# Kernel tuning notes

Hardware: AMD Instinct MI355X
Metric: run time of the kernel (lower is better)

Reference implementation:

```python
import jax, jax.numpy as jnp
import numpy as np

N, M, D = 8192, 8192, 64

def softplus(x):
    # transform_forward in pmf-automl
    return jnp.logaddexp(x, 0.0)

def inv_softplus(y):
    # transform_backward: log(exp(y) - 1), stable form
    return y + jnp.log(-jnp.expm1(-y))

def setup_inputs() -> dict:
    key = jax.random.key(0)
    k1, k2 = jax.random.split(key)
    X = jax.random.normal(k1, (N, D), dtype=jnp.float32)
    X2 = jax.random.normal(k2, (M, D), dtype=jnp.float32)
    # raw (pre-softplus) parameters, matching torch init: softplus(raw)=1
    lengthscale = jnp.full((1, D), inv_softplus(jnp.float32(1.0)), dtype=jnp.float32)
    variance = jnp.full((1,), inv_softplus(jnp.float32(1.0)), dtype=jnp.float32)
    return {"X": X, "X2": X2, "lengthscale": lengthscale, "variance": variance}

def reference(X, X2, lengthscale, variance):
    l = softplus(lengthscale)           # [1, D]
    v = softplus(variance)              # [1]
    Xl = X / l                          # [N, D]
    X2l = X2 / l                        # [M, D]
    xn = jnp.sum(Xl * Xl, axis=1)       # [N]
    yn = jnp.sum(X2l * X2l, axis=1)     # [M]
    cross = Xl @ X2l.T                  # [N, M]
    d2 = jnp.maximum(xn[:, None] + yn[None, :] - 2.0 * cross, 0.0)
    return v[0] * jnp.exp(-0.5 * d2)
```

## Files before the change

### kernel.cpp

```cpp
#include <hip/hip_runtime.h>
#include <math.h>

#define NN 8192
#define MM 8192
#define DD 64
#define BM 128
#define BN 128
#define LDS_S 132

__device__ __forceinline__ float softplus_f(float x) {
    return fmaxf(x, 0.0f) + log1pf(exp2f(-fabsf(x) * 1.4426950408889634f));
}

__global__ __launch_bounds__(256, 2)
void rbf_tile_kernel(const float* __restrict__ X, const float* __restrict__ X2,
                     const float* __restrict__ raw_l, const float* __restrict__ raw_v,
                     float* __restrict__ out) {
    __shared__ float As[DD][LDS_S];
    __shared__ float Bs[DD][LDS_S];
    __shared__ float xn[BM];
    __shared__ float yn[BN];

    const int t  = threadIdx.x;
    const int bn = blockIdx.x;
    const int bm = blockIdx.y;

    const int k4 = t & 15;
    const int r0 = t >> 4;

    float4 rl = ((const float4*)raw_l)[k4];
    const float il0 = 1.0f / softplus_f(rl.x);
    const float il1 = 1.0f / softplus_f(rl.y);
    const float il2 = 1.0f / softplus_f(rl.z);
    const float il3 = 1.0f / softplus_f(rl.w);

    const float* Xb  = X  + (size_t)(bm * BM) * DD;
    const float* X2b = X2 + (size_t)(bn * BN) * DD;

#pragma unroll
    for (int r = 0; r < 8; ++r) {
        const int row = r0 + 16 * r;
        float4 a = *(const float4*)(Xb + row * DD + 4 * k4);
        As[4 * k4 + 0][row] = a.x * il0;
        As[4 * k4 + 1][row] = a.y * il1;
        As[4 * k4 + 2][row] = a.z * il2;
        As[4 * k4 + 3][row] = a.w * il3;
        float4 b = *(const float4*)(X2b + row * DD + 4 * k4);
        Bs[4 * k4 + 0][row] = b.x * il0;
        Bs[4 * k4 + 1][row] = b.y * il1;
        Bs[4 * k4 + 2][row] = b.z * il2;
        Bs[4 * k4 + 3][row] = b.w * il3;
    }
    __syncthreads();

    {
        const int c = t & 127;
        float s = 0.0f;
        if (t < 128) {
#pragma unroll
            for (int k = 0; k < DD; ++k) { float a = As[k][c]; s = fmaf(a, a, s); }
            xn[c] = s;
        } else {
#pragma unroll
            for (int k = 0; k < DD; ++k) { float b = Bs[k][c]; s = fmaf(b, b, s); }
            yn[c] = s;
        }
    }
    __syncthreads();

    const int tx = t & 15;
    const int ty = t >> 4;

    float acc[2][4][2][4];
#pragma unroll
    for (int ii = 0; ii < 2; ++ii)
#pragma unroll
        for (int i = 0; i < 4; ++i)
#pragma unroll
            for (int jj = 0; jj < 2; ++jj)
#pragma unroll
                for (int j = 0; j < 4; ++j) acc[ii][i][jj][j] = 0.0f;

#pragma unroll 4
    for (int k = 0; k < DD; ++k) {
        float4 a0 = *(const float4*)&As[k][4 * ty];
        float4 a1 = *(const float4*)&As[k][4 * ty + 64];
        float4 b0 = *(const float4*)&Bs[k][4 * tx];
        float4 b1 = *(const float4*)&Bs[k][4 * tx + 64];
        float a[2][4] = {{a0.x, a0.y, a0.z, a0.w}, {a1.x, a1.y, a1.z, a1.w}};
        float b[2][4] = {{b0.x, b0.y, b0.z, b0.w}, {b1.x, b1.y, b1.z, b1.w}};
#pragma unroll
        for (int ii = 0; ii < 2; ++ii)
#pragma unroll
            for (int i = 0; i < 4; ++i)
#pragma unroll
                for (int jj = 0; jj < 2; ++jj)
#pragma unroll
                    for (int j = 0; j < 4; ++j)
                        acc[ii][i][jj][j] = fmaf(a[ii][i], b[jj][j], acc[ii][i][jj][j]);
    }

    const float v = softplus_f(raw_v[0]);
    const float c_exp = -0.5f * 1.4426950408889634f;

#pragma unroll
    for (int ii = 0; ii < 2; ++ii) {
#pragma unroll
        for (int i = 0; i < 4; ++i) {
            const int m = 4 * ty + 64 * ii + i;
            const float xnm = xn[m];
            float* orow = out + (size_t)(bm * BM + m) * MM + bn * BN;
#pragma unroll
            for (int jj = 0; jj < 2; ++jj) {
                const int n0 = 4 * tx + 64 * jj;
                float4 o;
                {
                    float d2 = fmaxf(xnm + yn[n0 + 0] - 2.0f * acc[ii][i][jj][0], 0.0f);
                    o.x = v * exp2f(c_exp * d2);
                }
                {
                    float d2 = fmaxf(xnm + yn[n0 + 1] - 2.0f * acc[ii][i][jj][1], 0.0f);
                    o.y = v * exp2f(c_exp * d2);
                }
                {
                    float d2 = fmaxf(xnm + yn[n0 + 2] - 2.0f * acc[ii][i][jj][2], 0.0f);
                    o.z = v * exp2f(c_exp * d2);
                }
                {
                    float d2 = fmaxf(xnm + yn[n0 + 3] - 2.0f * acc[ii][i][jj][3], 0.0f);
                    o.w = v * exp2f(c_exp * d2);
                }
                *(float4*)(orow + n0) = o;
            }
        }
    }
}

extern "C" void kernel_launch(void* const* d_in, const int* in_sizes, int n_in,
                              void* d_out, int out_size, void* d_ws, size_t ws_size,
                              hipStream_t stream) {
    const float* X     = (const float*)d_in[0];
    const float* X2    = (const float*)d_in[1];
    const float* raw_l = (const float*)d_in[2];
    const float* raw_v = (const float*)d_in[3];
    float* out = (float*)d_out;

    dim3 grid(MM / BN, NN / BM);
    dim3 block(256);
    rbf_tile_kernel<<<grid, block, 0, stream>>>(X, X2, raw_l, raw_v, out);
}
```

Before: 356.3 us.

## Compute cross term with split-bf16 MFMA instead of fp32 FMA

Replaces the scalar fp32 outer-product GEMM with bf16 MFMA 16x16x32 instructions. Operands are split into hi and lo bf16 parts and three products are accumulated to keep accuracy close to fp32. Row norms are now computed in fp32 straight from global memory, and the output layout changes to per-lane scalar stores. This trades 3x MFMA work and narrower, less coalesced stores for matrix-core throughput. The kernel is likely bound by the 256MB output write, so the gain may be limited.

```diff
diff --git a/kernel.cpp b/kernel.cpp
--- a/kernel.cpp
+++ b/kernel.cpp
@@ -6,18 +6,25 @@
 #define DD 64
 #define BM 128
 #define BN 128
-#define LDS_S 132
+#define STR 72
+
+typedef __bf16 bf16x8 __attribute__((ext_vector_type(8)));
+typedef __bf16 bf16x4 __attribute__((ext_vector_type(4)));
+typedef float f32x4 __attribute__((ext_vector_type(4)));
 
 __device__ __forceinline__ float softplus_f(float x) {
     return fmaxf(x, 0.0f) + log1pf(exp2f(-fabsf(x) * 1.4426950408889634f));
 }
 
 __global__ __launch_bounds__(256, 2)
-void rbf_tile_kernel(const float* __restrict__ X, const float* __restrict__ X2,
+void rbf_mfma_kernel(const float* __restrict__ X, const float* __restrict__ X2,
                      const float* __restrict__ raw_l, const float* __restrict__ raw_v,
                      float* __restrict__ out) {
-    __shared__ float As[DD][LDS_S];
-    __shared__ float Bs[DD][LDS_S];
+    __shared__ __bf16 Ah[BM][STR];
+    __shared__ __bf16 Al[BM][STR];
+    __shared__ __bf16 Bh[BN][STR];
+    __shared__ __bf16 Bl[BN][STR];
+    __shared__ float ls[DD];
     __shared__ float xn[BM];
     __shared__ float yn[BN];
 
@@ -25,14 +32,15 @@
     const int bn = blockIdx.x;
     const int bm = blockIdx.y;
 
+    if (t < DD) ls[t] = 1.0f / softplus_f(raw_l[t]);
+    __syncthreads();
+
     const int k4 = t & 15;
     const int r0 = t >> 4;
-
-    float4 rl = ((const float4*)raw_l)[k4];
-    const float il0 = 1.0f / softplus_f(rl.x);
-    const float il1 = 1.0f / softplus_f(rl.y);
-    const float il2 = 1.0f / softplus_f(rl.z);
-    const float il3 = 1.0f / softplus_f(rl.w);
+    const float il0 = ls[4 * k4 + 0];
+    const float il1 = ls[4 * k4 + 1];
+    const float il2 = ls[4 * k4 + 2];
+    const float il3 = ls[4 * k4 + 3];
 
     const float* Xb  = X  + (size_t)(bm * BM) * DD;
     const float* X2b = X2 + (size_t)(bn * BN) * DD;
@@ -40,97 +48,99 @@
 #pragma unroll
     for (int r = 0; r < 8; ++r) {
         const int row = r0 + 16 * r;
-        float4 a = *(const float4*)(Xb + row * DD + 4 * k4);
-        As[4 * k4 + 0][row] = a.x * il0;
-        As[4 * k4 + 1][row] = a.y * il1;
-        As[4 * k4 + 2][row] = a.z * il2;
-        As[4 * k4 + 3][row] = a.w * il3;
-        float4 b = *(const float4*)(X2b + row * DD + 4 * k4);
-        Bs[4 * k4 + 0][row] = b.x * il0;
-        Bs[4 * k4 + 1][row] = b.y * il1;
-        Bs[4 * k4 + 2][row] = b.z * il2;
-        Bs[4 * k4 + 3][row] = b.w * il3;
+        {
+            float4 a = *(const float4*)(Xb + row * DD + 4 * k4);
+            a.x *= il0; a.y *= il1; a.z *= il2; a.w *= il3;
+            bf16x4 h, l;
+            h[0] = (__bf16)a.x; l[0] = (__bf16)(a.x - (float)h[0]);
+            h[1] = (__bf16)a.y; l[1] = (__bf16)(a.y - (float)h[1]);
+            h[2] = (__bf16)a.z; l[2] = (__bf16)(a.z - (float)h[2]);
+            h[3] = (__bf16)a.w; l[3] = (__bf16)(a.w - (float)h[3]);
+            *(bf16x4*)&Ah[row][4 * k4] = h;
+            *(bf16x4*)&Al[row][4 * k4] = l;
+        }
+        {
+            float4 b = *(const float4*)(X2b + row * DD + 4 * k4);
+            b.x *= il0; b.y *= il1; b.z *= il2; b.w *= il3;
+            bf16x4 h, l;
+            h[0] = (__bf16)b.x; l[0] = (__bf16)(b.x - (float)h[0]);
+            h[1] = (__bf16)b.y; l[1] = (__bf16)(b.y - (float)h[1]);
+            h[2] = (__bf16)b.z; l[2] = (__bf16)(b.z - (float)h[2]);
+            h[3] = (__bf16)b.w; l[3] = (__bf16)(b.w - (float)h[3]);
+            *(bf16x4*)&Bh[row][4 * k4] = h;
+            *(bf16x4*)&Bl[row][4 * k4] = l;
+        }
+    }
+
+    {
+        const int rowl = t & 127;
+        const float* p = (t < 128) ? (Xb + rowl * DD) : (X2b + rowl * DD);
+        float s = 0.0f;
+#pragma unroll
+        for (int j = 0; j < 16; ++j) {
+            float4 a = *(const float4*)(p + 4 * j);
+            float e;
+            e = a.x * ls[4 * j + 0]; s = fmaf(e, e, s);
+            e = a.y * ls[4 * j + 1]; s = fmaf(e, e, s);
+            e = a.z * ls[4 * j + 2]; s = fmaf(e, e, s);
+            e = a.w * ls[4 * j + 3]; s = fmaf(e, e, s);
+        }
+        if (t < 128) xn[rowl] = s; else yn[rowl] = s;
     }
     __syncthreads();
 
-    {
-        const int c = t & 127;
-        float s = 0.0f;
-        if (t < 128) {
+    const int lane = t & 63;
+    const int q    = lane >> 4;
+    const int r16  = lane & 15;
+    const int w    = t >> 6;
+    const int row0 = (w >> 1) * 64;
+    const int col0 = (w & 1) * 64;
+
+    f32x4 acc[4][4];
 #pragma unroll
-            for (int k = 0; k < DD; ++k) { float a = As[k][c]; s = fmaf(a, a, s); }
-            xn[c] = s;
-        } else {
+    for (int mi = 0; mi < 4; ++mi)
 #pragma unroll
-            for (int k = 0; k < DD; ++k) { float b = Bs[k][c]; s = fmaf(b, b, s); }
-            yn[c] = s;
+        for (int ni = 0; ni < 4; ++ni)
+#pragma unroll
+            for (int r = 0; r < 4; ++r) acc[mi][ni][r] = 0.0f;
+
+#pragma unroll
+    for (int kc = 0; kc < 2; ++kc) {
+        const int k0 = kc * 32 + q * 8;
+        bf16x8 ah[4], al[4], bh[4], bl[4];
+#pragma unroll
+        for (int i = 0; i < 4; ++i) {
+            ah[i] = *(const bf16x8*)&Ah[row0 + i * 16 + r16][k0];
+            al[i] = *(const bf16x8*)&Al[row0 + i * 16 + r16][k0];
+            bh[i] = *(const bf16x8*)&Bh[col0 + i * 16 + r16][k0];
+            bl[i] = *(const bf16x8*)&Bl[col0 + i * 16 + r16][k0];
+        }
+#pragma unroll
+        for (int mi = 0; mi < 4; ++mi) {
+#pragma unroll
+            for (int ni = 0; ni < 4; ++ni) {
+                acc[mi][ni] = __builtin_amdgcn_mfma_f32_16x16x32_bf16(ah[mi], bh[ni], acc[mi][ni], 0, 0, 0);
+                acc[mi][ni] = __builtin_amdgcn_mfma_f32_16x16x32_bf16(ah[mi], bl[ni], acc[mi][ni], 0, 0, 0);
+                acc[mi][ni] = __builtin_amdgcn_mfma_f32_16x16x32_bf16(al[mi], bh[ni], acc[mi][ni], 0, 0, 0);
+            }
         }
     }
-    __syncthreads();
 
-    const int tx = t & 15;
-    const int ty = t >> 4;
-
-    float acc[2][4][2][4];
-#pragma unroll
-    for (int ii = 0; ii < 2; ++ii)
-#pragma unroll
-        for (int i = 0; i < 4; ++i)
-#pragma unroll
-            for (int jj = 0; jj < 2; ++jj)
-#pragma unroll
-                for (int j = 0; j < 4; ++j) acc[ii][i][jj][j] = 0.0f;
-
-#pragma unroll 4
-    for (int k = 0; k < DD; ++k) {
-        float4 a0 = *(const float4*)&As[k][4 * ty];
-        float4 a1 = *(const float4*)&As[k][4 * ty + 64];
-        float4 b0 = *(const float4*)&Bs[k][4 * tx];
-        float4 b1 = *(const float4*)&Bs[k][4 * tx + 64];
-        float a[2][4] = {{a0.x, a0.y, a0.z, a0.w}, {a1.x, a1.y, a1.z, a1.w}};
-        float b[2][4] = {{b0.x, b0.y, b0.z, b0.w}, {b1.x, b1.y, b1.z, b1.w}};
-#pragma unroll
-        for (int ii = 0; ii < 2; ++ii)
-#pragma unroll
-            for (int i = 0; i < 4; ++i)
-#pragma unroll
-                for (int jj = 0; jj < 2; ++jj)
-#pragma unroll
-                    for (int j = 0; j < 4; ++j)
-                        acc[ii][i][jj][j] = fmaf(a[ii][i], b[jj][j], acc[ii][i][jj][j]);
-    }
-
-    const float v = softplus_f(raw_v[0]);
-    const float c_exp = -0.5f * 1.4426950408889634f;
+    const float v  = softplus_f(raw_v[0]);
+    const float ce = -0.5f * 1.4426950408889634f;
 
 #pragma unroll
-    for (int ii = 0; ii < 2; ++ii) {
+    for (int mi = 0; mi < 4; ++mi) {
 #pragma unroll
-        for (int i = 0; i < 4; ++i) {
-            const int m = 4 * ty + 64 * ii + i;
-            const float xnm = xn[m];
-            float* orow = out + (size_t)(bm * BM + m) * MM + bn * BN;
+        for (int r = 0; r < 4; ++r) {
+            const int lrow = row0 + mi * 16 + q * 4 + r;
+            const float xr = xn[lrow];
+            float* orow = out + (size_t)(bm * BM + lrow) * MM + bn * BN;
 #pragma unroll
-            for (int jj = 0; jj < 2; ++jj) {
-                const int n0 = 4 * tx + 64 * jj;
-                float4 o;
-                {
-                    float d2 = fmaxf(xnm + yn[n0 + 0] - 2.0f * acc[ii][i][jj][0], 0.0f);
-                    o.x = v * exp2f(c_exp * d2);
-                }
-                {
-                    float d2 = fmaxf(xnm + yn[n0 + 1] - 2.0f * acc[ii][i][jj][1], 0.0f);
-                    o.y = v * exp2f(c_exp * d2);
-                }
-                {
-                    float d2 = fmaxf(xnm + yn[n0 + 2] - 2.0f * acc[ii][i][jj][2], 0.0f);
-                    o.z = v * exp2f(c_exp * d2);
-                }
-                {
-                    float d2 = fmaxf(xnm + yn[n0 + 3] - 2.0f * acc[ii][i][jj][3], 0.0f);
-                    o.w = v * exp2f(c_exp * d2);
-                }
-                *(float4*)(orow + n0) = o;
+            for (int ni = 0; ni < 4; ++ni) {
+                const int lcol = col0 + ni * 16 + r16;
+                float d2 = fmaxf(xr + yn[lcol] - 2.0f * acc[mi][ni][r], 0.0f);
+                orow[lcol] = v * exp2f(ce * d2);
             }
         }
     }
@@ -147,5 +157,5 @@
 
     dim3 grid(MM / BN, NN / BM);
     dim3 block(256);
-    rbf_tile_kernel<<<grid, block, 0, stream>>>(X, X2, raw_l, raw_v, out);
+    rbf_mfma_kernel<<<grid, block, 0, stream>>>(X, X2, raw_l, raw_v, out);
 }
```

New measurement: 325.7 us. 8.6% less time.
